# Performance work log

Measured on AMD Instinct MI355X. Metric: run time of the kernel, lower is better.

## Reference

```python
import jax, jax.numpy as jnp
import numpy as np

B, S, D = 2, 2048, 1024
N_EXP, TOP_K = 8, 2
CAP_FACTOR = 1.25

def setup_inputs() -> dict:
    key = jax.random.key(0)
    k1, k2 = jax.random.split(key)
    x = jax.random.normal(k1, (B, S, D), dtype=jnp.float32)
    W_gate = jax.random.normal(k2, (N_EXP, D), dtype=jnp.float32) * (1.0 / np.sqrt(D))
    return {"x": x, "W_gate": W_gate}

def reference(x, W_gate):
    Bq, Sq, d = x.shape
    N = Bq * Sq                      # num_tokens
    n_exp = W_gate.shape[0]
    top_k = TOP_K
    cap = int(N * top_k * CAP_FACTOR / n_exp)  # exp_capacity (static)

    x_flat = x.reshape(N, d)
    logits = x_flat @ W_gate.T                      # [N, n_exp]
    top_vals, top_idx = jax.lax.top_k(logits, top_k)  # [N, k]
    gates = jax.nn.softmax(top_vals, axis=-1)       # [N, k]

    # Serial token-major, k-minor assignment order == flatten row-major.
    e_flat = top_idx.reshape(-1)                    # [N*k]
    oh = jax.nn.one_hot(e_flat, n_exp, dtype=jnp.int32)
    # position within expert = # earlier slots routed to same expert
    pos = (jnp.cumsum(oh, axis=0) - oh)[jnp.arange(N * top_k), e_flat]
    pos_safe = jnp.where(pos < cap, pos, cap)       # cap -> out-of-bounds -> dropped

    tok = jnp.arange(N * top_k) // top_k            # owning token per slot
    g_flat = gates.reshape(-1)

    exp_mask = jnp.zeros((N, n_exp, cap), jnp.float32)
    exp_mask = exp_mask.at[tok, e_flat, pos_safe].set(g_flat, mode='drop')

    exp_batches = jnp.zeros((n_exp, cap, d), jnp.float32)
    exp_batches = exp_batches.at[e_flat, pos_safe].set(x_flat[tok], mode='drop')

    return gates, exp_mask, exp_batches
```

## Files before the change

kernel.cpp:

```cpp
#include <hip/hip_runtime.h>
#include <math.h>

#define NTOK   4096
#define DIM    1024
#define NEXP   8
#define CAP    1280
#define NSLOT  (NTOK*2)

#define OUT_MASK_OFF   ((size_t)NTOK*2)
#define OUT_BATCH_OFF  (OUT_MASK_OFF + (size_t)NTOK*NEXP*CAP)

__global__ __launch_bounds__(256) void gate_kernel(
    const float* __restrict__ x, const float* __restrict__ Wg,
    float* __restrict__ gates_out,
    int* __restrict__ e0a, int* __restrict__ e1a,
    float* __restrict__ g0a, float* __restrict__ g1a)
{
    const int t   = blockIdx.x;
    const int tid = threadIdx.x;

    const float4 xv = ((const float4*)(x + (size_t)t * DIM))[tid];

    float acc[NEXP];
#pragma unroll
    for (int e = 0; e < NEXP; ++e) {
        const float4 w = ((const float4*)(Wg + (size_t)e * DIM))[tid];
        acc[e] = xv.x * w.x + xv.y * w.y + xv.z * w.z + xv.w * w.w;
    }

#pragma unroll
    for (int off = 32; off >= 1; off >>= 1) {
#pragma unroll
        for (int e = 0; e < NEXP; ++e)
            acc[e] += __shfl_xor(acc[e], off);
    }

    __shared__ float red[4][NEXP];
    __shared__ float logits[NEXP];
    const int wave = tid >> 6;
    if ((tid & 63) == 0) {
#pragma unroll
        for (int e = 0; e < NEXP; ++e) red[wave][e] = acc[e];
    }
    __syncthreads();
    if (tid < NEXP) {
        logits[tid] = red[0][tid] + red[1][tid] + red[2][tid] + red[3][tid];
    }
    __syncthreads();

    if (tid == 0) {
        float best = -INFINITY, second = -INFINITY;
        int b0 = 0, b1 = 0;
#pragma unroll
        for (int e = 0; e < NEXP; ++e) {
            const float v = logits[e];
            if (v > best)        { second = best; b1 = b0; best = v; b0 = e; }
            else if (v > second) { second = v; b1 = e; }
        }
        const float e1v = __expf(second - best);
        const float inv = 1.0f / (1.0f + e1v);
        const float g0 = inv, g1 = e1v * inv;

        gates_out[(size_t)t * 2]     = g0;
        gates_out[(size_t)t * 2 + 1] = g1;
        e0a[t] = b0; e1a[t] = b1;
        g0a[t] = g0; g1a[t] = g1;
    }
}

__global__ __launch_bounds__(256) void scan_kernel(
    const int* __restrict__ e0a, const int* __restrict__ e1a,
    int* __restrict__ pos0a, int* __restrict__ pos1a,
    int* __restrict__ inv_out)
{
    __shared__ int cnt[256][NEXP + 1];
    __shared__ int invs[NEXP * CAP];

    const int tid = threadIdx.x;

    for (int i = tid; i < NEXP * CAP; i += 256) invs[i] = -1;

    const int tok0 = tid * 16;
    int ex[32];
    int local[NEXP];
#pragma unroll
    for (int e = 0; e < NEXP; ++e) local[e] = 0;
#pragma unroll
    for (int j = 0; j < 16; ++j) {
        const int a = e0a[tok0 + j];
        const int b = e1a[tok0 + j];
        ex[2 * j]     = a;
        ex[2 * j + 1] = b;
        local[a]++; local[b]++;
    }

    int val[NEXP];
#pragma unroll
    for (int e = 0; e < NEXP; ++e) { val[e] = local[e]; cnt[tid][e] = val[e]; }

    for (int off = 1; off < 256; off <<= 1) {
        __syncthreads();
        int nb[NEXP];
        const bool has = (tid >= off);
        if (has) {
#pragma unroll
            for (int e = 0; e < NEXP; ++e) nb[e] = cnt[tid - off][e];
        }
        __syncthreads();
        if (has) {
#pragma unroll
            for (int e = 0; e < NEXP; ++e) val[e] += nb[e];
        }
#pragma unroll
        for (int e = 0; e < NEXP; ++e) cnt[tid][e] = val[e];
    }
    __syncthreads();

    int run[NEXP];
#pragma unroll
    for (int e = 0; e < NEXP; ++e) run[e] = val[e] - local[e];

#pragma unroll
    for (int j = 0; j < 32; ++j) {
        const int e = ex[j];
        const int p = run[e]++;
        const int tok = tok0 + (j >> 1);
        if (j & 1) pos1a[tok] = p; else pos0a[tok] = p;
        if (p < CAP) invs[e * CAP + p] = tok;
    }
    __syncthreads();

    for (int i = tid; i < NEXP * CAP; i += 256) inv_out[i] = invs[i];
}

__global__ __launch_bounds__(256) void mask_kernel(
    const int* __restrict__ e0a, const int* __restrict__ e1a,
    const int* __restrict__ pos0a, const int* __restrict__ pos1a,
    const float* __restrict__ g0a, const float* __restrict__ g1a,
    float* __restrict__ mask_out)
{
    const int t   = blockIdx.x;
    const int tid = threadIdx.x;

    const int   e0 = e0a[t], e1 = e1a[t];
    const int   p0 = pos0a[t], p1 = pos1a[t];
    const float g0 = g0a[t],  g1 = g1a[t];

    float4* dst = (float4*)(mask_out + (size_t)t * NEXP * CAP);

#pragma unroll
    for (int i = 0; i < 10; ++i) {
        const int idx = tid + i * 256;
        const int e   = idx / (CAP / 4);
        const int c   = (idx - e * (CAP / 4)) * 4;

        float4 v = make_float4(0.f, 0.f, 0.f, 0.f);
        if (e == e0) {
            if (p0 == c)     v.x = g0;
            if (p0 == c + 1) v.y = g0;
            if (p0 == c + 2) v.z = g0;
            if (p0 == c + 3) v.w = g0;
        }
        if (e == e1) {
            if (p1 == c)     v.x = g1;
            if (p1 == c + 1) v.y = g1;
            if (p1 == c + 2) v.z = g1;
            if (p1 == c + 3) v.w = g1;
        }
        dst[idx] = v;
    }
}

__global__ __launch_bounds__(256) void batch_kernel(
    const int* __restrict__ inv, const float* __restrict__ x,
    float* __restrict__ batch_out)
{
    const int row = blockIdx.x;
    const int tid = threadIdx.x;
    const int tok = inv[row];

    float4 v = make_float4(0.f, 0.f, 0.f, 0.f);
    if (tok >= 0)
        v = ((const float4*)(x + (size_t)tok * DIM))[tid];

    ((float4*)(batch_out + (size_t)row * DIM))[tid] = v;
}

extern "C" void kernel_launch(void* const* d_in, const int* in_sizes, int n_in,
                              void* d_out, int out_size, void* d_ws, size_t ws_size,
                              hipStream_t stream)
{
    const float* x  = (const float*)d_in[0];
    const float* Wg = (const float*)d_in[1];

    float* out   = (float*)d_out;
    float* gates = out;
    float* mask  = out + OUT_MASK_OFF;
    float* batch = out + OUT_BATCH_OFF;

    int* wsi = (int*)d_ws;
    int*   e0a  = wsi;
    int*   e1a  = wsi + NTOK;
    float* g0a  = (float*)(wsi + 2 * NTOK);
    float* g1a  = (float*)(wsi + 3 * NTOK);
    int*   p0a  = wsi + 4 * NTOK;
    int*   p1a  = wsi + 5 * NTOK;
    int*   inv  = wsi + 6 * NTOK;

    gate_kernel <<<NTOK, 256, 0, stream>>>(x, Wg, gates, e0a, e1a, g0a, g1a);
    scan_kernel <<<1, 256, 0, stream>>>(e0a, e1a, p0a, p1a, inv);
    mask_kernel <<<NTOK, 256, 0, stream>>>(e0a, e1a, p0a, p1a, g0a, g1a, mask);
    batch_kernel<<<NEXP * CAP, 256, 0, stream>>>(inv, x, batch);
}
```

Before: 235.4 us.

## Fuse mask and batch writers, wave-per-token gating, shuffle-based packed scan

The gate kernel now assigns one wavefront per token, so the cross-wave LDS reduction and its barriers go away. The single-block scan switches from an LDS Hillis-Steele scan with many barriers to a wave shuffle scan over 16-bit packed counters, and uses vectorised int4 loads and stores. The mask and batch kernels are merged into one launch, with block ranges split between the two jobs, and both use nontemporal stores to cut launch count and cache pollution on the large output writes. The packed 16-bit counts assume per-expert totals stay below 65536, which holds for these sizes.

```diff
diff --git a/kernel.cpp b/kernel.cpp
--- a/kernel.cpp
+++ b/kernel.cpp
@@ -5,10 +5,11 @@
 #define DIM    1024
 #define NEXP   8
 #define CAP    1280
-#define NSLOT  (NTOK*2)
 
 #define OUT_MASK_OFF   ((size_t)NTOK*2)
 #define OUT_BATCH_OFF  (OUT_MASK_OFF + (size_t)NTOK*NEXP*CAP)
+
+typedef float f4 __attribute__((ext_vector_type(4)));
 
 __global__ __launch_bounds__(256) void gate_kernel(
     const float* __restrict__ x, const float* __restrict__ Wg,
@@ -16,16 +17,26 @@
     int* __restrict__ e0a, int* __restrict__ e1a,
     float* __restrict__ g0a, float* __restrict__ g1a)
 {
-    const int t   = blockIdx.x;
-    const int tid = threadIdx.x;
-
-    const float4 xv = ((const float4*)(x + (size_t)t * DIM))[tid];
+    const int wave = threadIdx.x >> 6;
+    const int lane = threadIdx.x & 63;
+    const int t    = blockIdx.x * 4 + wave;
+
+    const f4* xr = (const f4*)(x + (size_t)t * DIM);
+    f4 xv[4];
+#pragma unroll
+    for (int p = 0; p < 4; ++p) xv[p] = xr[p * 64 + lane];
 
     float acc[NEXP];
 #pragma unroll
     for (int e = 0; e < NEXP; ++e) {
-        const float4 w = ((const float4*)(Wg + (size_t)e * DIM))[tid];
-        acc[e] = xv.x * w.x + xv.y * w.y + xv.z * w.z + xv.w * w.w;
+        const f4* wr = (const f4*)(Wg + (size_t)e * DIM);
+        float a = 0.f;
+#pragma unroll
+        for (int p = 0; p < 4; ++p) {
+            const f4 w = wr[p * 64 + lane];
+            a += xv[p].x * w.x + xv[p].y * w.y + xv[p].z * w.z + xv[p].w * w.w;
+        }
+        acc[e] = a;
     }
 
 #pragma unroll
@@ -35,25 +46,12 @@
             acc[e] += __shfl_xor(acc[e], off);
     }
 
-    __shared__ float red[4][NEXP];
-    __shared__ float logits[NEXP];
-    const int wave = tid >> 6;
-    if ((tid & 63) == 0) {
-#pragma unroll
-        for (int e = 0; e < NEXP; ++e) red[wave][e] = acc[e];
-    }
-    __syncthreads();
-    if (tid < NEXP) {
-        logits[tid] = red[0][tid] + red[1][tid] + red[2][tid] + red[3][tid];
-    }
-    __syncthreads();
-
-    if (tid == 0) {
+    if (lane == 0) {
         float best = -INFINITY, second = -INFINITY;
         int b0 = 0, b1 = 0;
 #pragma unroll
         for (int e = 0; e < NEXP; ++e) {
-            const float v = logits[e];
+            const float v = acc[e];
             if (v > best)        { second = best; b1 = b0; best = v; b0 = e; }
             else if (v > second) { second = v; b1 = e; }
         }
@@ -73,117 +71,148 @@
     int* __restrict__ pos0a, int* __restrict__ pos1a,
     int* __restrict__ inv_out)
 {
-    __shared__ int cnt[256][NEXP + 1];
     __shared__ int invs[NEXP * CAP];
-
-    const int tid = threadIdx.x;
+    __shared__ unsigned wtot[4][4];
+
+    const int tid  = threadIdx.x;
+    const int wave = tid >> 6;
+    const int lane = tid & 63;
 
     for (int i = tid; i < NEXP * CAP; i += 256) invs[i] = -1;
 
     const int tok0 = tid * 16;
-    int ex[32];
+    int ea[16], eb[16];
+    {
+        const int4* va = (const int4*)(e0a + tok0);
+        const int4* vb = (const int4*)(e1a + tok0);
+#pragma unroll
+        for (int q = 0; q < 4; ++q) {
+            int4 a = va[q], b = vb[q];
+            ea[4*q] = a.x; ea[4*q+1] = a.y; ea[4*q+2] = a.z; ea[4*q+3] = a.w;
+            eb[4*q] = b.x; eb[4*q+1] = b.y; eb[4*q+2] = b.z; eb[4*q+3] = b.w;
+        }
+    }
+
     int local[NEXP];
 #pragma unroll
     for (int e = 0; e < NEXP; ++e) local[e] = 0;
 #pragma unroll
+    for (int j = 0; j < 16; ++j) { local[ea[j]]++; local[eb[j]]++; }
+
+    unsigned pk[4];
+#pragma unroll
+    for (int q = 0; q < 4; ++q)
+        pk[q] = (unsigned)local[2*q] | ((unsigned)local[2*q+1] << 16);
+    const unsigned my0 = pk[0], my1 = pk[1], my2 = pk[2], my3 = pk[3];
+
+#pragma unroll
+    for (int off = 1; off < 64; off <<= 1) {
+        unsigned n0 = __shfl_up((int)pk[0], off);
+        unsigned n1 = __shfl_up((int)pk[1], off);
+        unsigned n2 = __shfl_up((int)pk[2], off);
+        unsigned n3 = __shfl_up((int)pk[3], off);
+        if (lane >= off) { pk[0] += n0; pk[1] += n1; pk[2] += n2; pk[3] += n3; }
+    }
+
+    if (lane == 63) {
+#pragma unroll
+        for (int q = 0; q < 4; ++q) wtot[wave][q] = pk[q];
+    }
+    __syncthreads();
+
+#pragma unroll
+    for (int w = 0; w < 4; ++w) {
+        if (w < wave) {
+            pk[0] += wtot[w][0]; pk[1] += wtot[w][1];
+            pk[2] += wtot[w][2]; pk[3] += wtot[w][3];
+        }
+    }
+    pk[0] -= my0; pk[1] -= my1; pk[2] -= my2; pk[3] -= my3;
+
+    int run[NEXP];
+#pragma unroll
+    for (int q = 0; q < 4; ++q) {
+        run[2*q]   = (int)(pk[q] & 0xFFFFu);
+        run[2*q+1] = (int)(pk[q] >> 16);
+    }
+
+    int p0r[16], p1r[16];
+#pragma unroll
     for (int j = 0; j < 16; ++j) {
-        const int a = e0a[tok0 + j];
-        const int b = e1a[tok0 + j];
-        ex[2 * j]     = a;
-        ex[2 * j + 1] = b;
-        local[a]++; local[b]++;
-    }
-
-    int val[NEXP];
-#pragma unroll
-    for (int e = 0; e < NEXP; ++e) { val[e] = local[e]; cnt[tid][e] = val[e]; }
-
-    for (int off = 1; off < 256; off <<= 1) {
-        __syncthreads();
-        int nb[NEXP];
-        const bool has = (tid >= off);
-        if (has) {
-#pragma unroll
-            for (int e = 0; e < NEXP; ++e) nb[e] = cnt[tid - off][e];
-        }
-        __syncthreads();
-        if (has) {
-#pragma unroll
-            for (int e = 0; e < NEXP; ++e) val[e] += nb[e];
-        }
-#pragma unroll
-        for (int e = 0; e < NEXP; ++e) cnt[tid][e] = val[e];
+        const int tok = tok0 + j;
+        int e = ea[j];
+        int p = run[e]++;
+        p0r[j] = p;
+        if (p < CAP) invs[e * CAP + p] = tok;
+        e = eb[j];
+        p = run[e]++;
+        p1r[j] = p;
+        if (p < CAP) invs[e * CAP + p] = tok;
+    }
+
+#pragma unroll
+    for (int q = 0; q < 4; ++q) {
+        ((int4*)(pos0a + tok0))[q] = make_int4(p0r[4*q], p0r[4*q+1], p0r[4*q+2], p0r[4*q+3]);
+        ((int4*)(pos1a + tok0))[q] = make_int4(p1r[4*q], p1r[4*q+1], p1r[4*q+2], p1r[4*q+3]);
     }
     __syncthreads();
 
-    int run[NEXP];
-#pragma unroll
-    for (int e = 0; e < NEXP; ++e) run[e] = val[e] - local[e];
-
-#pragma unroll
-    for (int j = 0; j < 32; ++j) {
-        const int e = ex[j];
-        const int p = run[e]++;
-        const int tok = tok0 + (j >> 1);
-        if (j & 1) pos1a[tok] = p; else pos0a[tok] = p;
-        if (p < CAP) invs[e * CAP + p] = tok;
-    }
-    __syncthreads();
-
-    for (int i = tid; i < NEXP * CAP; i += 256) inv_out[i] = invs[i];
-}
-
-__global__ __launch_bounds__(256) void mask_kernel(
+    for (int i = tid; i < NEXP * CAP / 4; i += 256)
+        ((int4*)inv_out)[i] = ((const int4*)invs)[i];
+}
+
+#define BATCH_BLOCKS 2560
+__global__ __launch_bounds__(256) void writer_kernel(
     const int* __restrict__ e0a, const int* __restrict__ e1a,
     const int* __restrict__ pos0a, const int* __restrict__ pos1a,
     const float* __restrict__ g0a, const float* __restrict__ g1a,
-    float* __restrict__ mask_out)
-{
-    const int t   = blockIdx.x;
+    const int* __restrict__ inv, const float* __restrict__ x,
+    float* __restrict__ mask_out, float* __restrict__ batch_out)
+{
     const int tid = threadIdx.x;
 
-    const int   e0 = e0a[t], e1 = e1a[t];
-    const int   p0 = pos0a[t], p1 = pos1a[t];
-    const float g0 = g0a[t],  g1 = g1a[t];
-
-    float4* dst = (float4*)(mask_out + (size_t)t * NEXP * CAP);
-
-#pragma unroll
-    for (int i = 0; i < 10; ++i) {
-        const int idx = tid + i * 256;
-        const int e   = idx / (CAP / 4);
-        const int c   = (idx - e * (CAP / 4)) * 4;
-
-        float4 v = make_float4(0.f, 0.f, 0.f, 0.f);
-        if (e == e0) {
-            if (p0 == c)     v.x = g0;
-            if (p0 == c + 1) v.y = g0;
-            if (p0 == c + 2) v.z = g0;
-            if (p0 == c + 3) v.w = g0;
-        }
-        if (e == e1) {
-            if (p1 == c)     v.x = g1;
-            if (p1 == c + 1) v.y = g1;
-            if (p1 == c + 2) v.z = g1;
-            if (p1 == c + 3) v.w = g1;
-        }
-        dst[idx] = v;
-    }
-}
-
-__global__ __launch_bounds__(256) void batch_kernel(
-    const int* __restrict__ inv, const float* __restrict__ x,
-    float* __restrict__ batch_out)
-{
-    const int row = blockIdx.x;
-    const int tid = threadIdx.x;
-    const int tok = inv[row];
-
-    float4 v = make_float4(0.f, 0.f, 0.f, 0.f);
-    if (tok >= 0)
-        v = ((const float4*)(x + (size_t)tok * DIM))[tid];
-
-    ((float4*)(batch_out + (size_t)row * DIM))[tid] = v;
+    if (blockIdx.x < BATCH_BLOCKS) {
+        const int base = blockIdx.x * 4;
+#pragma unroll
+        for (int i = 0; i < 4; ++i) {
+            const int row = base + i;
+            const int tok = inv[row];
+            f4 v = (f4)(0.f);
+            if (tok >= 0)
+                v = ((const f4*)(x + (size_t)tok * DIM))[tid];
+            __builtin_nontemporal_store(v, (f4*)(batch_out + (size_t)row * DIM) + tid);
+        }
+    } else {
+        const int t = blockIdx.x - BATCH_BLOCKS;
+
+        const int   e0 = e0a[t], e1 = e1a[t];
+        const int   p0 = pos0a[t], p1 = pos1a[t];
+        const float g0 = g0a[t],  g1 = g1a[t];
+
+        f4* dst = (f4*)(mask_out + (size_t)t * NEXP * CAP);
+
+#pragma unroll
+        for (int i = 0; i < 10; ++i) {
+            const int idx = tid + i * 256;
+            const int e   = idx / (CAP / 4);
+            const int c   = (idx - e * (CAP / 4)) * 4;
+
+            f4 v = (f4)(0.f);
+            if (e == e0) {
+                if (p0 == c)     v.x = g0;
+                if (p0 == c + 1) v.y = g0;
+                if (p0 == c + 2) v.z = g0;
+                if (p0 == c + 3) v.w = g0;
+            }
+            if (e == e1) {
+                if (p1 == c)     v.x = g1;
+                if (p1 == c + 1) v.y = g1;
+                if (p1 == c + 2) v.z = g1;
+                if (p1 == c + 3) v.w = g1;
+            }
+            __builtin_nontemporal_store(v, dst + idx);
+        }
+    }
 }
 
 extern "C" void kernel_launch(void* const* d_in, const int* in_sizes, int n_in,
@@ -207,8 +236,8 @@
     int*   p1a  = wsi + 5 * NTOK;
     int*   inv  = wsi + 6 * NTOK;
 
-    gate_kernel <<<NTOK, 256, 0, stream>>>(x, Wg, gates, e0a, e1a, g0a, g1a);
-    scan_kernel <<<1, 256, 0, stream>>>(e0a, e1a, p0a, p1a, inv);
-    mask_kernel <<<NTOK, 256, 0, stream>>>(e0a, e1a, p0a, p1a, g0a, g1a, mask);
-    batch_kernel<<<NEXP * CAP, 256, 0, stream>>>(inv, x, batch);
-}
+    gate_kernel  <<<NTOK / 4, 256, 0, stream>>>(x, Wg, gates, e0a, e1a, g0a, g1a);
+    scan_kernel  <<<1, 256, 0, stream>>>(e0a, e1a, p0a, p1a, inv);
+    writer_kernel<<<BATCH_BLOCKS + NTOK, 256, 0, stream>>>(
+        e0a, e1a, p0a, p1a, g0a, g1a, inv, x, mask, batch);
+}
```

New measurement: 238.5 us. About the same (+1.3%).
